# Kernel tuning notes

Hardware: AMD Instinct MI355X
Metric: run time of the kernel (lower is better)

## Reference

```python
import jax, jax.numpy as jnp
import numpy as np

D_Z, D_Y, N, N_SAMPLE = 512, 32, 2048, 128
JITTER = 0.0001


def setup_inputs() -> dict:
    key = jax.random.key(0)
    k1, k2, k3, k4, k5 = jax.random.split(key, 5)
    d_total = D_Z + N * D_Y
    return {
        "m": jax.random.normal(k1, (d_total,), jnp.float32),
        "Lz": jax.random.normal(k2, (D_Z, D_Z), jnp.float32),
        "Ly_blocks": jax.random.normal(k3, (N, D_Y, D_Y), jnp.float32),
        "Lyz": jax.random.normal(k4, (N * D_Y, D_Z), jnp.float32),
        "eps": jax.random.normal(k5, (N_SAMPLE, d_total), jnp.float32),
    }


def reference(m, Lz, Ly_blocks, Lyz, eps):
    # L_dense (block lower-triangular) is never materialized; we compute
    # z = m + eps @ L_dense.T block-wise. L_dense = [[tril(Lz), 0], [Lyz, blkdiag(tril(Ly_n))]] + jitter*I.
    dt = Lz.dtype
    Lz_t = jnp.tril(Lz) + JITTER * jnp.eye(D_Z, dtype=dt)
    Ly = jnp.tril(Ly_blocks) + JITTER * jnp.eye(D_Y, dtype=dt)  # [N, d_y, d_y]

    eps_z = eps[:, :D_Z]                          # [S, d_z]
    eps_y = eps[:, D_Z:].reshape(-1, N, D_Y)      # [S, N, d_y]

    z_z = m[:D_Z] + eps_z @ Lz_t.T                # [S, d_z]
    cross = eps_z @ Lyz.T                         # [S, N*d_y]
    diag = jnp.einsum("snj,nij->sni", eps_y, Ly).reshape(-1, N * D_Y)
    z_y = m[D_Z:] + cross + diag                  # [S, N*d_y]
    return jnp.concatenate([z_z, z_y], axis=1)
```

## Files before the change

kernel.cpp:

```cpp
#include <hip/hip_runtime.h>

#define DZ 512
#define DT 66048
#define NTILE 2064
#define SV_JITTER 1e-4f

typedef __attribute__((ext_vector_type(8))) short bf8;
typedef __attribute__((ext_vector_type(4))) short bf4;
typedef __attribute__((ext_vector_type(4))) float f4;

#define BAR()                                                   \
  do {                                                          \
    __builtin_amdgcn_sched_barrier(0);                          \
    asm volatile("s_waitcnt lgkmcnt(0)" ::: "memory");          \
    __builtin_amdgcn_s_barrier();                               \
    __builtin_amdgcn_sched_barrier(0);                          \
  } while (0)

__device__ __forceinline__ short f2bf(float f) {
  unsigned u = __builtin_bit_cast(unsigned, f);
  return (short)((u + 0x7FFFu + ((u >> 16) & 1u)) >> 16);
}

__device__ __forceinline__ bf8 cvt8(f4 a, f4 b) {
  bf8 r = { f2bf(a[0]), f2bf(a[1]), f2bf(a[2]), f2bf(a[3]),
            f2bf(b[0]), f2bf(b[1]), f2bf(b[2]), f2bf(b[3]) };
  return r;
}

__device__ __forceinline__ bf8 cvt8_tril(f4 x, f4 y, int kbase, int diag) {
  bf8 r;
  #pragma unroll
  for (int t = 0; t < 8; ++t) {
    const int k = kbase + t;
    const float vt = (t < 4) ? x[t] : y[t - 4];
    const float val = (k < diag) ? vt : ((k == diag) ? vt + SV_JITTER : 0.f);
    r[t] = f2bf(val);
  }
  return r;
}

__global__ __launch_bounds__(512, 2)
void sv_kernel(const float* __restrict__ mv, const float* __restrict__ Lz,
               const float* __restrict__ Ly, const float* __restrict__ Lyz,
               const float* __restrict__ eps, float* __restrict__ out) {
  __shared__ short Afrag[128 * 512];
  __shared__ short Bpan[32 * 512];

  const int tid = threadIdx.x;
  const int lane = tid & 63;
  const int wv = tid >> 6;
  const int lcol = lane & 15;
  const int q = lane >> 4;
  const int b = blockIdx.x;

  f4 sv[8];
  auto stage_load = [&](int T) {
    const float* Ls = (T < 16) ? (Lz + (size_t)(32 * T) * DZ)
                               : (Lyz + (size_t)(32 * T - DZ) * DZ);
    #pragma unroll
    for (int i = 0; i < 8; ++i)
      sv[i] = *(const f4*)(Ls + (size_t)4 * (i * 512 + tid));
  };
  auto stage_write = [&](int T) {
    #pragma unroll
    for (int i = 0; i < 8; ++i) {
      const int f = i * 512 + tid;
      const int ro = f >> 7;
      const int c4 = f & 127;
      bf4 w;
      if (T < 16) {
        const int gcol = 32 * T + ro;
        #pragma unroll
        for (int t = 0; t < 4; ++t) {
          const int k = 4 * c4 + t;
          const float val =
              (k < gcol) ? sv[i][t] : ((k == gcol) ? sv[i][t] + SV_JITTER : 0.f);
          w[t] = f2bf(val);
        }
      } else {
        #pragma unroll
        for (int t = 0; t < 4; ++t) w[t] = f2bf(sv[i][t]);
      }
      const int off = (ro << 10) + ((((c4 >> 1) ^ (ro & 7))) << 4) + ((c4 & 1) << 3);
      *(bf4*)((char*)Bpan + off) = w;
    }
  };
  auto readB = [&](int g, int kk) -> bf8 {
    const int R = 16 * g + lcol;
    const int off = (R << 10) + (((4 * kk + q) ^ (R & 7)) << 4);
    return *(const bf8*)((const char*)Bpan + off);
  };

  stage_load(b);
  {
    const int slot = lane;
    const int r0 = wv * 16;
    #pragma unroll 4
    for (int i = 0; i < 16; ++i) {
      const int r = r0 + i;
      const float* p = eps + (size_t)(16 * (r & 7) + (slot & 15)) * DT +
                       (r >> 3) * 32 + (slot >> 4) * 8;
      const f4 x = *(const f4*)p;
      const f4 y = *(const f4*)(p + 4);
      *(bf8*)&Afrag[r * 512 + slot * 8] = cvt8(x, y);
    }
  }
  stage_write(b);
  BAR();

  #pragma unroll 1
  for (int r = 0; r < 9; ++r) {
    const int T = r * 256 + b;
    if (T >= NTILE) break;
    const bool isz = (T < 16);
    const int Tn = T + 256;
    const bool have_next = (Tn < NTILE);

    if (have_next) stage_load(Tn);

    f4 dax, day, db0x, db0y, db1x, db1y;
    if (!isz) {
      const int nb = T - 16;
      const float* pa =
          eps + (size_t)(16 * wv + lcol) * DT + DZ + (size_t)nb * 32 + 8 * q;
      dax = *(const f4*)pa; day = *(const f4*)(pa + 4);
      const float* pb0 = Ly + ((size_t)nb * 32 + lcol) * 32 + 8 * q;
      db0x = *(const f4*)pb0; db0y = *(const f4*)(pb0 + 4);
      const float* pb1 = Ly + ((size_t)nb * 32 + 16 + lcol) * 32 + 8 * q;
      db1x = *(const f4*)pb1; db1y = *(const f4*)(pb1 + 4);
    }

    f4 acc0 = f4{0.f, 0.f, 0.f, 0.f};
    f4 acc1 = f4{0.f, 0.f, 0.f, 0.f};
    #pragma unroll
    for (int kk = 0; kk < 16; ++kk) {
      const bf8 af = *(const bf8*)&Afrag[(kk * 8 + wv) * 512 + lane * 8];
      const bf8 b0 = readB(0, kk);
      const bf8 b1 = readB(1, kk);
      acc0 = __builtin_amdgcn_mfma_f32_16x16x32_bf16(af, b0, acc0, 0, 0, 0);
      acc1 = __builtin_amdgcn_mfma_f32_16x16x32_bf16(af, b1, acc1, 0, 0, 0);
    }
    if (!isz) {
      const bf8 afd = cvt8(dax, day);
      const bf8 dbf0 = cvt8_tril(db0x, db0y, 8 * q, lcol);
      const bf8 dbf1 = cvt8_tril(db1x, db1y, 8 * q, 16 + lcol);
      acc0 = __builtin_amdgcn_mfma_f32_16x16x32_bf16(afd, dbf0, acc0, 0, 0, 0);
      acc1 = __builtin_amdgcn_mfma_f32_16x16x32_bf16(afd, dbf1, acc1, 0, 0, 0);
    }

    {
      const int c0 = 32 * T + lcol;
      const float m0 = mv[c0], m1 = mv[c0 + 16];
      #pragma unroll
      for (int rr = 0; rr < 4; ++rr) {
        const size_t rowoff = (size_t)(16 * wv + 4 * q + rr) * DT;
        out[rowoff + c0] = acc0[rr] + m0;
        out[rowoff + c0 + 16] = acc1[rr] + m1;
      }
    }

    BAR();
    if (have_next) stage_write(Tn);
    BAR();
  }
}

extern "C" void kernel_launch(void* const* d_in, const int* in_sizes, int n_in,
                              void* d_out, int out_size, void* d_ws, size_t ws_size,
                              hipStream_t stream) {
  const float* m   = (const float*)d_in[0];
  const float* Lz  = (const float*)d_in[1];
  const float* Ly  = (const float*)d_in[2];
  const float* Lyz = (const float*)d_in[3];
  const float* eps = (const float*)d_in[4];
  float* out = (float*)d_out;
  sv_kernel<<<dim3(256), dim3(512), 0, stream>>>(m, Lz, Ly, Lyz, eps, out);
}
```

Baseline: 51.17 us.

## Split work into 512 smaller blocks over sample halves and 16-column tiles

Changes the decomposition from 256 blocks of 512 threads (all 128 samples × 32 columns per tile) to 512 blocks of 256 threads, each covering 64 samples × 16 columns. The aim is to fill more CUs on the 256-CU part and shrink per-block LDS, allowing more blocks to be resident. In exchange, each B panel of Lz/Lyz is loaded and converted twice, once per sample half, and each wave issues one MFMA chain instead of two, which lowers per-wave instruction-level parallelism.

```diff
diff --git a/kernel.cpp b/kernel.cpp
--- a/kernel.cpp
+++ b/kernel.cpp
@@ -2,7 +2,7 @@
 
 #define DZ 512
 #define DT 66048
-#define NTILE 2064
+#define NT 4128
 #define SV_JITTER 1e-4f
 
 typedef __attribute__((ext_vector_type(8))) short bf8;
@@ -40,12 +40,12 @@
   return r;
 }
 
-__global__ __launch_bounds__(512, 2)
+__global__ __launch_bounds__(256, 2)
 void sv_kernel(const float* __restrict__ mv, const float* __restrict__ Lz,
                const float* __restrict__ Ly, const float* __restrict__ Lyz,
                const float* __restrict__ eps, float* __restrict__ out) {
-  __shared__ short Afrag[128 * 512];
-  __shared__ short Bpan[32 * 512];
+  __shared__ short Afrag[64 * 512];
+  __shared__ short Bpan[16 * 512];
 
   const int tid = threadIdx.x;
   const int lane = tid & 63;
@@ -53,24 +53,27 @@
   const int lcol = lane & 15;
   const int q = lane >> 4;
   const int b = blockIdx.x;
+  const int half = b >> 8;
+  const int bcol = b & 255;
+  const int srow0 = 64 * half;
 
   f4 sv[8];
   auto stage_load = [&](int T) {
-    const float* Ls = (T < 16) ? (Lz + (size_t)(32 * T) * DZ)
-                               : (Lyz + (size_t)(32 * T - DZ) * DZ);
+    const float* Ls = (T < 32) ? (Lz + (size_t)(16 * T) * DZ)
+                               : (Lyz + (size_t)(16 * T) * DZ - (size_t)DZ * DZ);
     #pragma unroll
     for (int i = 0; i < 8; ++i)
-      sv[i] = *(const f4*)(Ls + (size_t)4 * (i * 512 + tid));
+      sv[i] = *(const f4*)(Ls + (size_t)4 * (i * 256 + tid));
   };
   auto stage_write = [&](int T) {
     #pragma unroll
     for (int i = 0; i < 8; ++i) {
-      const int f = i * 512 + tid;
+      const int f = i * 256 + tid;
       const int ro = f >> 7;
       const int c4 = f & 127;
       bf4 w;
-      if (T < 16) {
-        const int gcol = 32 * T + ro;
+      if (T < 32) {
+        const int gcol = 16 * T + ro;
         #pragma unroll
         for (int t = 0; t < 4; ++t) {
           const int k = 4 * c4 + t;
@@ -86,77 +89,69 @@
       *(bf4*)((char*)Bpan + off) = w;
     }
   };
-  auto readB = [&](int g, int kk) -> bf8 {
-    const int R = 16 * g + lcol;
-    const int off = (R << 10) + (((4 * kk + q) ^ (R & 7)) << 4);
+  auto readB = [&](int kk) -> bf8 {
+    const int off = (lcol << 10) + (((4 * kk + q) ^ (lcol & 7)) << 4);
     return *(const bf8*)((const char*)Bpan + off);
   };
 
-  stage_load(b);
+  stage_load(bcol);
   {
     const int slot = lane;
-    const int r0 = wv * 16;
     #pragma unroll 4
     for (int i = 0; i < 16; ++i) {
-      const int r = r0 + i;
-      const float* p = eps + (size_t)(16 * (r & 7) + (slot & 15)) * DT +
-                       (r >> 3) * 32 + (slot >> 4) * 8;
+      const int r = wv * 16 + i;
+      const int mi = r & 3, kk = r >> 2;
+      const float* p = eps + (size_t)(srow0 + 16 * mi + (slot & 15)) * DT +
+                       kk * 32 + (slot >> 4) * 8;
       const f4 x = *(const f4*)p;
       const f4 y = *(const f4*)(p + 4);
       *(bf8*)&Afrag[r * 512 + slot * 8] = cvt8(x, y);
     }
   }
-  stage_write(b);
+  stage_write(bcol);
   BAR();
 
   #pragma unroll 1
-  for (int r = 0; r < 9; ++r) {
-    const int T = r * 256 + b;
-    if (T >= NTILE) break;
-    const bool isz = (T < 16);
+  for (int r = 0; r < 17; ++r) {
+    const int T = bcol + 256 * r;
+    if (T >= NT) break;
+    const bool isz = (T < 32);
     const int Tn = T + 256;
-    const bool have_next = (Tn < NTILE);
+    const bool have_next = (Tn < NT);
 
     if (have_next) stage_load(Tn);
 
-    f4 dax, day, db0x, db0y, db1x, db1y;
+    f4 dax, day, dbx, dby;
+    int dI = 0;
     if (!isz) {
-      const int nb = T - 16;
+      const int nb = (T - 32) >> 1;
+      dI = (T & 1) * 16;
       const float* pa =
-          eps + (size_t)(16 * wv + lcol) * DT + DZ + (size_t)nb * 32 + 8 * q;
+          eps + (size_t)(srow0 + 16 * wv + lcol) * DT + DZ + (size_t)nb * 32 + 8 * q;
       dax = *(const f4*)pa; day = *(const f4*)(pa + 4);
-      const float* pb0 = Ly + ((size_t)nb * 32 + lcol) * 32 + 8 * q;
-      db0x = *(const f4*)pb0; db0y = *(const f4*)(pb0 + 4);
-      const float* pb1 = Ly + ((size_t)nb * 32 + 16 + lcol) * 32 + 8 * q;
-      db1x = *(const f4*)pb1; db1y = *(const f4*)(pb1 + 4);
+      const float* pb = Ly + ((size_t)nb * 32 + dI + lcol) * 32 + 8 * q;
+      dbx = *(const f4*)pb; dby = *(const f4*)(pb + 4);
     }
 
-    f4 acc0 = f4{0.f, 0.f, 0.f, 0.f};
-    f4 acc1 = f4{0.f, 0.f, 0.f, 0.f};
+    f4 acc = f4{0.f, 0.f, 0.f, 0.f};
     #pragma unroll
     for (int kk = 0; kk < 16; ++kk) {
-      const bf8 af = *(const bf8*)&Afrag[(kk * 8 + wv) * 512 + lane * 8];
-      const bf8 b0 = readB(0, kk);
-      const bf8 b1 = readB(1, kk);
-      acc0 = __builtin_amdgcn_mfma_f32_16x16x32_bf16(af, b0, acc0, 0, 0, 0);
-      acc1 = __builtin_amdgcn_mfma_f32_16x16x32_bf16(af, b1, acc1, 0, 0, 0);
+      const bf8 af = *(const bf8*)&Afrag[(kk * 4 + wv) * 512 + lane * 8];
+      const bf8 bf = readB(kk);
+      acc = __builtin_amdgcn_mfma_f32_16x16x32_bf16(af, bf, acc, 0, 0, 0);
     }
     if (!isz) {
       const bf8 afd = cvt8(dax, day);
-      const bf8 dbf0 = cvt8_tril(db0x, db0y, 8 * q, lcol);
-      const bf8 dbf1 = cvt8_tril(db1x, db1y, 8 * q, 16 + lcol);
-      acc0 = __builtin_amdgcn_mfma_f32_16x16x32_bf16(afd, dbf0, acc0, 0, 0, 0);
-      acc1 = __builtin_amdgcn_mfma_f32_16x16x32_bf16(afd, dbf1, acc1, 0, 0, 0);
+      const bf8 dbf = cvt8_tril(dbx, dby, 8 * q, dI + lcol);
+      acc = __builtin_amdgcn_mfma_f32_16x16x32_bf16(afd, dbf, acc, 0, 0, 0);
     }
 
     {
-      const int c0 = 32 * T + lcol;
-      const float m0 = mv[c0], m1 = mv[c0 + 16];
+      const int c0 = 16 * T + lcol;
+      const float m0 = mv[c0];
       #pragma unroll
       for (int rr = 0; rr < 4; ++rr) {
-        const size_t rowoff = (size_t)(16 * wv + 4 * q + rr) * DT;
-        out[rowoff + c0] = acc0[rr] + m0;
-        out[rowoff + c0 + 16] = acc1[rr] + m1;
+        out[(size_t)(srow0 + 16 * wv + 4 * q + rr) * DT + c0] = acc[rr] + m0;
       }
     }
 
@@ -175,5 +170,5 @@
   const float* Lyz = (const float*)d_in[3];
   const float* eps = (const float*)d_in[4];
   float* out = (float*)d_out;
-  sv_kernel<<<dim3(256), dim3(512), 0, stream>>>(m, Lz, Ly, Lyz, eps, out);
+  sv_kernel<<<dim3(512), dim3(256), 0, stream>>>(m, Lz, Ly, Lyz, eps, out);
 }
```

After: 58.06 us. +13.4%, slower.

## Precompute bf16 eps_z fragments once and stream them into LDS directly

Applied to the files above, without the earlier changes.

Adds a small pre-kernel that converts the shared eps_z block to bf16 in MFMA fragment order and stores it in a workspace. The main kernel then loads it into LDS with global_load_lds instead of having each of 256 blocks reread strided fp32 eps and convert it. This removes redundant strided global reads and conversion work from every block's prologue. The cost is an extra kernel launch plus a dependency between the two launches, and it only takes effect when the workspace is large enough.

```diff
diff --git a/kernel.cpp b/kernel.cpp
--- a/kernel.cpp
+++ b/kernel.cpp
@@ -8,6 +8,8 @@
 typedef __attribute__((ext_vector_type(8))) short bf8;
 typedef __attribute__((ext_vector_type(4))) short bf4;
 typedef __attribute__((ext_vector_type(4))) float f4;
+typedef __attribute__((address_space(1))) const void glb_t;
+typedef __attribute__((address_space(3))) void lds_t;
 
 #define BAR()                                                   \
   do {                                                          \
@@ -40,10 +42,24 @@
   return r;
 }
 
+__global__ __launch_bounds__(256)
+void eps_conv_kernel(const float* __restrict__ eps, short* __restrict__ ws) {
+  const int g = blockIdx.x * 256 + threadIdx.x;
+  const int r = g >> 6;
+  const int slot = g & 63;
+  const float* p = eps + (size_t)(16 * (r & 7) + (slot & 15)) * DT +
+                   (r >> 3) * 32 + (slot >> 4) * 8;
+  const f4 x = *(const f4*)p;
+  const f4 y = *(const f4*)(p + 4);
+  *(bf8*)&ws[r * 512 + slot * 8] = cvt8(x, y);
+}
+
+template <bool USE_WS>
 __global__ __launch_bounds__(512, 2)
 void sv_kernel(const float* __restrict__ mv, const float* __restrict__ Lz,
                const float* __restrict__ Ly, const float* __restrict__ Lyz,
-               const float* __restrict__ eps, float* __restrict__ out) {
+               const float* __restrict__ eps, float* __restrict__ out,
+               const short* __restrict__ aws) {
   __shared__ short Afrag[128 * 512];
   __shared__ short Bpan[32 * 512];
 
@@ -93,12 +109,18 @@
   };
 
   stage_load(b);
-  {
+  if constexpr (USE_WS) {
+    #pragma unroll
+    for (int i = 0; i < 16; ++i) {
+      const int r = wv * 16 + i;
+      __builtin_amdgcn_global_load_lds((glb_t*)(aws + r * 512 + lane * 8),
+                                       (lds_t*)(&Afrag[r * 512]), 16, 0, 0);
+    }
+  } else {
     const int slot = lane;
-    const int r0 = wv * 16;
     #pragma unroll 4
     for (int i = 0; i < 16; ++i) {
-      const int r = r0 + i;
+      const int r = wv * 16 + i;
       const float* p = eps + (size_t)(16 * (r & 7) + (slot & 15)) * DT +
                        (r >> 3) * 32 + (slot >> 4) * 8;
       const f4 x = *(const f4*)p;
@@ -107,6 +129,7 @@
     }
   }
   stage_write(b);
+  asm volatile("s_waitcnt vmcnt(0)" ::: "memory");
   BAR();
 
   #pragma unroll 1
@@ -175,5 +198,13 @@
   const float* Lyz = (const float*)d_in[3];
   const float* eps = (const float*)d_in[4];
   float* out = (float*)d_out;
-  sv_kernel<<<dim3(256), dim3(512), 0, stream>>>(m, Lz, Ly, Lyz, eps, out);
-}
+  if (ws_size >= 128 * 512 * sizeof(short)) {
+    short* aws = (short*)d_ws;
+    eps_conv_kernel<<<dim3(32), dim3(256), 0, stream>>>(eps, aws);
+    sv_kernel<true><<<dim3(256), dim3(512), 0, stream>>>(m, Lz, Ly, Lyz, eps,
+                                                         out, aws);
+  } else {
+    sv_kernel<false><<<dim3(256), dim3(512), 0, stream>>>(m, Lz, Ly, Lyz, eps,
+                                                          out, nullptr);
+  }
+}
```

Result: slower. 110.2 us (+115.3%).
